# Kernel optimization log

Hardware: AMD Instinct MI355X
Metric: run time of the kernel (lower is better)

Reference implementation:

```python
import jax, jax.numpy as jnp
import numpy as np

B, C, H, W = 8, 192, 120, 120
WSIZES = [4, 8, 12]
BN_EPS = 1e-5


def _conv1x1(t, w, b):
    # t: [b,c,h,w], w: [o,c], b: [o]
    return jnp.einsum('oc,bchw->bohw', w, t) + b[None, :, None, None]


def _bn(t, g, bb, m, v):
    scale = (g * jax.lax.rsqrt(v + BN_EPS))[None, :, None, None]
    return (t - m[None, :, None, None]) * scale + bb[None, :, None, None]


def _partition_qv(t, ws):
    # t: [b, 2c, h, w] -> qx, vx each [b*nh*nw, ws*ws, c]
    b, c2, h, w = t.shape
    c = c2 // 2
    nh, nw = h // ws, w // ws
    t = t.reshape(b, 2, c, nh, ws, nw, ws)
    t = t.transpose(1, 0, 3, 5, 4, 6, 2).reshape(2, b * nh * nw, ws * ws, c)
    return t[0], t[1]


def _merge(t, ws, b, h, w):
    # t: [b*nh*nw, ws*ws, c] -> [b, c, h, w]
    nh, nw = h // ws, w // ws
    c = t.shape[-1]
    t = t.reshape(b, nh, nw, ws, ws, c)
    return t.transpose(0, 5, 1, 3, 2, 4).reshape(b, c, h, w)


def setup_inputs() -> dict:
    key = jax.random.key(0)
    ks = jax.random.split(key, 6)
    d = {}
    d['x'] = jax.random.normal(ks[0], (B, C, H, W), jnp.float32)
    d['y'] = jax.random.normal(ks[1], (B, C, H, W), jnp.float32)
    d['w_in'] = jax.random.normal(ks[2], (2 * C, C), jnp.float32) * 0.05
    d['b_in'] = jax.random.normal(ks[3], (2 * C,), jnp.float32) * 0.01
    d['bn_gamma'] = jnp.ones((2 * C,), jnp.float32)
    d['bn_beta'] = jnp.zeros((2 * C,), jnp.float32)
    d['bn_mean'] = jnp.zeros((2 * C,), jnp.float32)
    d['bn_var'] = jnp.ones((2 * C,), jnp.float32)
    d['w_out'] = jax.random.normal(ks[4], (C, C), jnp.float32) * 0.05
    d['b_out'] = jax.random.normal(ks[5], (C,), jnp.float32) * 0.01
    return d


def reference(x, y, w_in, b_in, bn_gamma, bn_beta, bn_mean, bn_var, w_out, b_out):
    b, c, h, w = x.shape
    xp = _bn(_conv1x1(x, w_in, b_in), bn_gamma, bn_beta, bn_mean, bn_var)
    yp = _bn(_conv1x1(y, w_in, b_in), bn_gamma, bn_beta, bn_mean, bn_var)
    chunk = c * 2 // 3
    y1s, atns = [], []
    for i, ws in enumerate(WSIZES):
        x_ = xp[:, i * chunk:(i + 1) * chunk]
        y_ = yp[:, i * chunk:(i + 1) * chunk]
        s = ws // 2  # shifts > 0 -> shifted windows
        x_ = jnp.roll(x_, (-s, -s), axis=(2, 3))
        y_ = jnp.roll(y_, (-s, -s), axis=(2, 3))
        qx, vx = _partition_qv(x_, ws)
        qy, vy = _partition_qv(y_, ws)
        atn = jax.nn.softmax(jnp.einsum('nqc,nkc->nqk', qx, qy), axis=-1)
        o = jnp.einsum('nqk,nkc->nqc', atn, vx)
        o = _merge(o, ws, b, h, w)
        o = jnp.roll(o, (s, s), axis=(2, 3))
        y1s.append(o)
        atns.append(atn)
    y1 = _conv1x1(jnp.concatenate(y1s, axis=1), w_out, b_out)
    return (y1, atns[0], atns[1], atns[2])
```

## Files before the change

kernel.cpp:

```cpp
#include <hip/hip_runtime.h>

typedef __bf16 bf16x8 __attribute__((ext_vector_type(8)));
typedef float f32x4 __attribute__((ext_vector_type(4)));
typedef float f32x2 __attribute__((ext_vector_type(2)));
typedef unsigned int u32x4 __attribute__((ext_vector_type(4)));
typedef unsigned int u32x2 __attribute__((ext_vector_type(2)));

#define HW 14400
#define CIN 192

__device__ __forceinline__ unsigned short f2bf(float f) {
  unsigned int u = __builtin_bit_cast(unsigned int, f);
  u = (u + 0x7FFFu + ((u >> 16) & 1u)) >> 16;
  return (unsigned short)u;
}
__device__ __forceinline__ float bf2f(unsigned short h) {
  unsigned int u = ((unsigned int)h) << 16;
  return __builtin_bit_cast(float, u);
}

__global__ void prep_kernel(const float* __restrict__ w_in, const float* __restrict__ b_in,
                            const float* __restrict__ g, const float* __restrict__ be,
                            const float* __restrict__ mu, const float* __restrict__ va,
                            const float* __restrict__ w_out,
                            unsigned short* __restrict__ wx, unsigned short* __restrict__ wy,
                            unsigned short* __restrict__ wo,
                            float* __restrict__ bx, float* __restrict__ by) {
  int idx = blockIdx.x * 256 + threadIdx.x;
  if (idx < 384 * 192) {
    int o = idx / 192;
    float s = g[o] * rsqrtf(va[o] + 1e-5f);
    wx[idx] = f2bf(w_in[idx] * s);
  } else if (idx < 384 * 192 + 192 * 192) {
    int j = idx - 384 * 192;
    int jo = j / 192, c = j % 192;
    int o = (jo >> 6) * 128 + (jo & 63);
    float s = g[o] * rsqrtf(va[o] + 1e-5f);
    wy[j] = f2bf(w_in[o * 192 + c] * s);
  } else if (idx < 384 * 192 + 2 * 192 * 192) {
    int j = idx - (384 * 192 + 192 * 192);
    int o = j / 192, cs = j % 192;
    int s = cs & 63;
    int src = (cs & ~63) | ((s & 3) * 16 + (s >> 2));
    wo[j] = f2bf(w_out[o * 192 + src]);
  }
  if (idx < 384) {
    float s = g[idx] * rsqrtf(va[idx] + 1e-5f);
    bx[idx] = (b_in[idx] - mu[idx]) * s + be[idx];
  } else if (idx < 384 + 192) {
    int jo = idx - 384;
    int o = (jo >> 6) * 128 + (jo & 63);
    float s = g[o] * rsqrtf(va[o] + 1e-5f);
    by[jo] = (b_in[o] - mu[o]) * s + be[o];
  }
}

template <int NOUT>
__launch_bounds__(384, 2)
__global__ void conv_in_kernel(const float* __restrict__ X,
                               const unsigned short* __restrict__ Wb,
                               const float* __restrict__ bias,
                               unsigned short* __restrict__ Out) {
  constexpr int M = (NOUT == 384) ? 4 : 2;
  __shared__ unsigned short a_lds[2][64 * 40];
  const int t = threadIdx.x;
  const int wave = t >> 6, lane = t & 63, l15 = lane & 15, l4 = lane >> 4;
  const int wchunk = (NOUT == 384) ? wave : (wave >> 1);
  const int px_base = (NOUT == 384) ? 0 : ((wave & 1) * 32);
  const int wo0 = wchunk * 64;
  const int b = blockIdx.x / 225;
  const int px0 = (blockIdx.x % 225) * 64;
  const float* Xb = X + (size_t)b * CIN * HW + px0;

  f32x4 acc[M][4];
#pragma unroll
  for (int n = 0; n < 4; ++n) {
    float bv = bias[wo0 + n * 16 + l15];
#pragma unroll
    for (int m = 0; m < M; ++m) acc[m][n] = f32x4{bv, bv, bv, bv};
  }

  const int c_off = (t & 7) * 4, px2 = ((t >> 3) & 31) * 2;
  auto stage = [&](int kc, int buf) {
    if (t < 256) {
      const float* src = Xb + (size_t)(kc * 32 + c_off) * HW + px2;
      f32x2 v0 = *reinterpret_cast<const f32x2*>(src);
      f32x2 v1 = *reinterpret_cast<const f32x2*>(src + HW);
      f32x2 v2 = *reinterpret_cast<const f32x2*>(src + 2 * HW);
      f32x2 v3 = *reinterpret_cast<const f32x2*>(src + 3 * HW);
      u32x2 r0 = {(unsigned)f2bf(v0[0]) | ((unsigned)f2bf(v1[0]) << 16),
                  (unsigned)f2bf(v2[0]) | ((unsigned)f2bf(v3[0]) << 16)};
      u32x2 r1 = {(unsigned)f2bf(v0[1]) | ((unsigned)f2bf(v1[1]) << 16),
                  (unsigned)f2bf(v2[1]) | ((unsigned)f2bf(v3[1]) << 16)};
      *reinterpret_cast<u32x2*>(&a_lds[buf][px2 * 40 + c_off]) = r0;
      *reinterpret_cast<u32x2*>(&a_lds[buf][(px2 + 1) * 40 + c_off]) = r1;
    }
  };
  auto loadW = [&](int kc, int n) {
    return *reinterpret_cast<const bf16x8*>(
        Wb + (size_t)(wo0 + n * 16 + l15) * CIN + kc * 32 + l4 * 8);
  };

  stage(0, 0);
  bf16x8 bw[4], bwn[4];
#pragma unroll
  for (int n = 0; n < 4; ++n) bw[n] = loadW(0, n);

  for (int kc = 0; kc < 6; ++kc) {
    __syncthreads();
    if (kc < 5) {
      stage(kc + 1, (kc + 1) & 1);
#pragma unroll
      for (int n = 0; n < 4; ++n) bwn[n] = loadW(kc + 1, n);
    }
    bf16x8 af[M];
#pragma unroll
    for (int m = 0; m < M; ++m)
      af[m] = *reinterpret_cast<const bf16x8*>(
          &a_lds[kc & 1][(px_base + m * 16 + l15) * 40 + l4 * 8]);
#pragma unroll
    for (int n = 0; n < 4; ++n)
#pragma unroll
      for (int m = 0; m < M; ++m)
        acc[m][n] = __builtin_amdgcn_mfma_f32_16x16x32_bf16(af[m], bw[n], acc[m][n], 0, 0, 0);
#pragma unroll
    for (int n = 0; n < 4; ++n) bw[n] = bwn[n];
  }

#pragma unroll
  for (int m = 0; m < M; ++m) {
#pragma unroll
    for (int r = 0; r < 4; ++r) {
      int px = px_base + m * 16 + l4 * 4 + r;
      u32x2 pk = {(unsigned)f2bf(acc[m][0][r]) | ((unsigned)f2bf(acc[m][1][r]) << 16),
                  (unsigned)f2bf(acc[m][2][r]) | ((unsigned)f2bf(acc[m][3][r]) << 16)};
      *reinterpret_cast<u32x2*>(Out + ((size_t)b * HW + px0 + px) * NOUT + wo0 + l15 * 4) = pk;
    }
  }
}

template <int WS, int SI, int NTHR>
__launch_bounds__(NTHR, 2)
__global__ void attn_kernel(const unsigned short* __restrict__ XP,
                            const unsigned short* __restrict__ YQ,
                            unsigned short* __restrict__ Z,
                            float* __restrict__ ATN) {
  constexpr int S = WS / 2, L = WS * WS, NH = 120 / WS, TT = L / 16;
  constexpr int NWAVE = NTHR / 64;
  constexpr int SMAX = (TT + NWAVE - 1) / NWAVE;
  constexpr int KP = ((L + 31) / 32) * 32;
  constexpr int PL = KP + 8;
  constexpr int KSTEPS = KP / 32;
  constexpr int POOLE = (L * 72 > L * PL) ? L * 72 : L * PL;
  __shared__ unsigned short pool[POOLE];
  __shared__ unsigned short vt_lds[64 * PL];
  unsigned short* k_lds = pool;
  unsigned short* p_lds = pool;

  const int t = threadIdx.x;
  const int win = blockIdx.x;
  const int b = win / (NH * NH);
  const int r_ = win % (NH * NH);
  const int ih = r_ / NH, iw = r_ % NH;
  const int wave = t >> 6, lane = t & 63, l15 = lane & 15, l4 = lane >> 4;

  auto pixof = [&](int e) {
    int p = e / WS, qc = e % WS;
    int h = ih * WS + p + S; if (h >= 120) h -= 120;
    int w = iw * WS + qc + S; if (w >= 120) w -= 120;
    return b * HW + h * 120 + w;
  };

  for (int idx = t; idx < L * 8; idx += NTHR) {
    int e = idx >> 3, c8 = (idx & 7) * 8;
    *reinterpret_cast<u32x4*>(&k_lds[e * 72 + c8]) =
        *reinterpret_cast<const u32x4*>(YQ + (size_t)pixof(e) * 192 + SI * 64 + c8);
  }
  for (int idx = t; idx < L * 8; idx += NTHR) {
    int e = idx >> 3, c8 = (idx & 7) * 8;
    u32x4 v = *reinterpret_cast<const u32x4*>(XP + (size_t)pixof(e) * 384 + SI * 128 + 64 + c8);
    const unsigned short* vh = reinterpret_cast<const unsigned short*>(&v);
#pragma unroll
    for (int j = 0; j < 8; ++j) vt_lds[(c8 + j) * PL + e] = vh[j];
  }
  if constexpr (KP > L) {
    for (int idx = t; idx < 64 * (KP - L); idx += NTHR)
      vt_lds[(idx / (KP - L)) * PL + L + (idx % (KP - L))] = 0;
  }

  bf16x8 af[SMAX][2];
#pragma unroll
  for (int si = 0; si < SMAX; ++si) {
    int ti = wave + si * NWAVE;
    if (ti < TT) {
      const unsigned short* qp =
          XP + (size_t)pixof(ti * 16 + l15) * 384 + SI * 128 + l4 * 8;
      af[si][0] = *reinterpret_cast<const bf16x8*>(qp);
      af[si][1] = *reinterpret_cast<const bf16x8*>(qp + 32);
    }
  }
  __syncthreads();

  f32x4 sacc[SMAX][TT];
#pragma unroll
  for (int si = 0; si < SMAX; ++si)
#pragma unroll
    for (int tj = 0; tj < TT; ++tj) sacc[si][tj] = f32x4{0.f, 0.f, 0.f, 0.f};
#pragma unroll
  for (int tj = 0; tj < TT; ++tj) {
    bf16x8 b0 = *reinterpret_cast<const bf16x8*>(&k_lds[(tj * 16 + l15) * 72 + l4 * 8]);
    bf16x8 b1 = *reinterpret_cast<const bf16x8*>(&k_lds[(tj * 16 + l15) * 72 + 32 + l4 * 8]);
#pragma unroll
    for (int si = 0; si < SMAX; ++si) {
      int ti = wave + si * NWAVE;
      if (ti < TT) {
        sacc[si][tj] = __builtin_amdgcn_mfma_f32_16x16x32_bf16(af[si][0], b0, sacc[si][tj], 0, 0, 0);
        sacc[si][tj] = __builtin_amdgcn_mfma_f32_16x16x32_bf16(af[si][1], b1, sacc[si][tj], 0, 0, 0);
      }
    }
  }

  float inv_[SMAX][4];
#pragma unroll
  for (int si = 0; si < SMAX; ++si) {
    int ti = wave + si * NWAVE;
    if (ti < TT) {
#pragma unroll
      for (int r = 0; r < 4; ++r) {
        float m = -1e30f;
#pragma unroll
        for (int tj = 0; tj < TT; ++tj) m = fmaxf(m, sacc[si][tj][r]);
#pragma unroll
        for (int mk = 1; mk < 16; mk <<= 1) m = fmaxf(m, __shfl_xor(m, mk, 64));
        float s = 0.f;
#pragma unroll
        for (int tj = 0; tj < TT; ++tj) {
          float e = __expf(sacc[si][tj][r] - m);
          sacc[si][tj][r] = e;
          s += e;
        }
#pragma unroll
        for (int mk = 1; mk < 16; mk <<= 1) s += __shfl_xor(s, mk, 64);
        inv_[si][r] = 1.f / s;
      }
    }
  }

  __syncthreads();

  if constexpr (KP > L) {
#pragma unroll
    for (int si = 0; si < SMAX; ++si) {
      int ti = wave + si * NWAVE;
      if (ti < TT)
        *reinterpret_cast<unsigned long long*>(
            &p_lds[(ti * 16 + l15) * PL + L + l4 * 4]) = 0ULL;
    }
  }

  float* aout = ATN + (size_t)win * L * L;
#pragma unroll
  for (int si = 0; si < SMAX; ++si) {
    int ti = wave + si * NWAVE;
    if (ti < TT) {
#pragma unroll
      for (int tj = 0; tj < TT; ++tj)
#pragma unroll
        for (int r = 0; r < 4; ++r) {
          float p = sacc[si][tj][r] * inv_[si][r];
          int row = ti * 16 + l4 * 4 + r, col = tj * 16 + l15;
          aout[row * L + col] = p;
          p_lds[row * PL + col] = f2bf(p);
        }
    }
  }
  __syncthreads();

#pragma unroll
  for (int si = 0; si < SMAX; ++si) {
    int ti = wave + si * NWAVE;
    if (ti < TT) {
      bf16x8 ap[KSTEPS];
#pragma unroll
      for (int kk = 0; kk < KSTEPS; ++kk)
        ap[kk] = *reinterpret_cast<const bf16x8*>(&p_lds[(ti * 16 + l15) * PL + kk * 32 + l4 * 8]);
      int opix[4];
#pragma unroll
      for (int r = 0; r < 4; ++r) opix[r] = pixof(ti * 16 + l4 * 4 + r);
#pragma unroll
      for (int cj = 0; cj < 4; ++cj) {
        f32x4 o = {0.f, 0.f, 0.f, 0.f};
#pragma unroll
        for (int kk = 0; kk < KSTEPS; ++kk) {
          bf16x8 bv = *reinterpret_cast<const bf16x8*>(&vt_lds[(cj * 16 + l15) * PL + kk * 32 + l4 * 8]);
          o = __builtin_amdgcn_mfma_f32_16x16x32_bf16(ap[kk], bv, o, 0, 0, 0);
        }
#pragma unroll
        for (int r = 0; r < 4; ++r)
          Z[(size_t)opix[r] * 192 + SI * 64 + cj * 16 + l15] = f2bf(o[r]);
      }
    }
  }
}

__launch_bounds__(256, 2)
__global__ void conv_out_kernel(const unsigned short* __restrict__ Z,
                                const unsigned short* __restrict__ Wo,
                                const float* __restrict__ bout,
                                float* __restrict__ Y1) {
  __shared__ unsigned short z_lds[64 * 40];
  __shared__ unsigned short w_lds[192 * 40];
  __shared__ float ep[4][48 * 68];
  const int t = threadIdx.x, wave = t >> 6, lane = t & 63;
  const int l15 = lane & 15, l4 = lane >> 4;
  const int b = blockIdx.x / 225, px0 = (blockIdx.x % 225) * 64;
  const unsigned short* Zb = Z + ((size_t)b * HW + px0) * 192;
  const int wo0 = wave * 48;
  f32x4 acc[3][4];
#pragma unroll
  for (int m = 0; m < 3; ++m) {
    f32x4 bv;
#pragma unroll
    for (int r = 0; r < 4; ++r) bv[r] = bout[wo0 + m * 16 + l4 * 4 + r];
#pragma unroll
    for (int n = 0; n < 4; ++n) acc[m][n] = bv;
  }
  for (int kc = 0; kc < 6; ++kc) {
    const int c0 = kc * 32;
    {
      int px = t >> 2, c8 = (t & 3) * 8;
      *reinterpret_cast<u32x4*>(&z_lds[px * 40 + c8]) =
          *reinterpret_cast<const u32x4*>(Zb + (size_t)px * 192 + c0 + c8);
    }
#pragma unroll
    for (int p = 0; p < 3; ++p) {
      int o = p * 64 + (t >> 2), c8 = (t & 3) * 8;
      *reinterpret_cast<u32x4*>(&w_lds[o * 40 + c8]) =
          *reinterpret_cast<const u32x4*>(Wo + (size_t)o * 192 + c0 + c8);
    }
    __syncthreads();
    bf16x8 bfr[4];
#pragma unroll
    for (int n = 0; n < 4; ++n)
      bfr[n] = *reinterpret_cast<const bf16x8*>(&z_lds[(n * 16 + l15) * 40 + l4 * 8]);
#pragma unroll
    for (int m = 0; m < 3; ++m) {
      bf16x8 af = *reinterpret_cast<const bf16x8*>(&w_lds[(wo0 + m * 16 + l15) * 40 + l4 * 8]);
#pragma unroll
      for (int n = 0; n < 4; ++n)
        acc[m][n] = __builtin_amdgcn_mfma_f32_16x16x32_bf16(af, bfr[n], acc[m][n], 0, 0, 0);
    }
    __syncthreads();
  }

  float* sl = ep[wave];
#pragma unroll
  for (int m = 0; m < 3; ++m)
#pragma unroll
    for (int n = 0; n < 4; ++n)
#pragma unroll
      for (int r = 0; r < 4; ++r)
        sl[(m * 16 + l4 * 4 + r) * 68 + n * 16 + l15] = acc[m][n][r];

  float* Yb = Y1 + (size_t)b * 192 * HW + px0;
#pragma unroll
  for (int i = 0; i < 3; ++i) {
    int row = i * 16 + (lane >> 2);
    int col0 = (lane & 3) * 16;
#pragma unroll
    for (int q = 0; q < 4; ++q) {
      f32x4 vv = *reinterpret_cast<const f32x4*>(&sl[row * 68 + col0 + q * 4]);
      *reinterpret_cast<f32x4*>(Yb + (size_t)(wo0 + row) * HW + col0 + q * 4) = vv;
    }
  }
}

extern "C" void kernel_launch(void* const* d_in, const int* in_sizes, int n_in,
                              void* d_out, int out_size, void* d_ws, size_t ws_size,
                              hipStream_t stream) {
  const float* x = (const float*)d_in[0];
  const float* y = (const float*)d_in[1];
  const float* w_in = (const float*)d_in[2];
  const float* b_in = (const float*)d_in[3];
  const float* g = (const float*)d_in[4];
  const float* be = (const float*)d_in[5];
  const float* mu = (const float*)d_in[6];
  const float* va = (const float*)d_in[7];
  const float* w_out = (const float*)d_in[8];
  const float* b_out = (const float*)d_in[9];
  char* ws = (char*)d_ws;
  unsigned short* wx = (unsigned short*)(ws + 0);
  unsigned short* wy = (unsigned short*)(ws + 147456);
  unsigned short* wo = (unsigned short*)(ws + 221184);
  float* bx = (float*)(ws + 294912);
  float* by = (float*)(ws + 296448);
  unsigned short* xp = (unsigned short*)(ws + 297216);
  unsigned short* yq = (unsigned short*)(ws + 297216 + (size_t)115200 * 384 * 2);
  unsigned short* z  = (unsigned short*)(ws + 297216 + (size_t)115200 * 384 * 2 +
                                         (size_t)115200 * 192 * 2);
  float* out = (float*)d_out;

  prep_kernel<<<576, 256, 0, stream>>>(w_in, b_in, g, be, mu, va, w_out, wx, wy, wo, bx, by);
  conv_in_kernel<384><<<1800, 384, 0, stream>>>(x, wx, bx, xp);
  conv_in_kernel<192><<<1800, 384, 0, stream>>>(y, wy, by, yq);
  attn_kernel<4, 0, 64><<<7200, 64, 0, stream>>>(xp, yq, z, out + 22118400);
  attn_kernel<8, 1, 256><<<1800, 256, 0, stream>>>(xp, yq, z, out + 23961600);
  attn_kernel<12, 2, 256><<<800, 256, 0, stream>>>(xp, yq, z, out + 31334400);
  conv_out_kernel<<<1800, 256, 0, stream>>>(z, wo, b_out, out);
}
```

Measured before the change: 277.5 us.

## Stage full input tile once in conv_in and drop LDS epilogue in conv_out

conv_in now loads the whole 192-channel by 64-pixel input tile up front with 16-byte vector loads, converts it to bf16 into a single large LDS buffer, and synchronises once. This replaces the per-k-chunk double-buffered staging and its per-iteration barriers. conv_out stops transposing results through an LDS scratch area and writes accumulators directly to global memory in 64-byte row segments. The trade-offs are more LDS and registers per block in conv_in, scalar 2-byte LDS stores that may hit bank conflicts, and less coalesced global stores in conv_out.

```diff
diff --git a/kernel.cpp b/kernel.cpp
--- a/kernel.cpp
+++ b/kernel.cpp
@@ -2,7 +2,6 @@
 
 typedef __bf16 bf16x8 __attribute__((ext_vector_type(8)));
 typedef float f32x4 __attribute__((ext_vector_type(4)));
-typedef float f32x2 __attribute__((ext_vector_type(2)));
 typedef unsigned int u32x4 __attribute__((ext_vector_type(4)));
 typedef unsigned int u32x2 __attribute__((ext_vector_type(2)));
 
@@ -62,7 +61,7 @@
                                const float* __restrict__ bias,
                                unsigned short* __restrict__ Out) {
   constexpr int M = (NOUT == 384) ? 4 : 2;
-  __shared__ unsigned short a_lds[2][64 * 40];
+  __shared__ unsigned short a_lds[64 * 200];
   const int t = threadIdx.x;
   const int wave = t >> 6, lane = t & 63, l15 = lane & 15, l4 = lane >> 4;
   const int wchunk = (NOUT == 384) ? wave : (wave >> 1);
@@ -72,44 +71,44 @@
   const int px0 = (blockIdx.x % 225) * 64;
   const float* Xb = X + (size_t)b * CIN * HW + px0;
 
-  f32x4 acc[M][4];
-#pragma unroll
-  for (int n = 0; n < 4; ++n) {
-    float bv = bias[wo0 + n * 16 + l15];
-#pragma unroll
-    for (int m = 0; m < M; ++m) acc[m][n] = f32x4{bv, bv, bv, bv};
-  }
-
-  const int c_off = (t & 7) * 4, px2 = ((t >> 3) & 31) * 2;
-  auto stage = [&](int kc, int buf) {
-    if (t < 256) {
-      const float* src = Xb + (size_t)(kc * 32 + c_off) * HW + px2;
-      f32x2 v0 = *reinterpret_cast<const f32x2*>(src);
-      f32x2 v1 = *reinterpret_cast<const f32x2*>(src + HW);
-      f32x2 v2 = *reinterpret_cast<const f32x2*>(src + 2 * HW);
-      f32x2 v3 = *reinterpret_cast<const f32x2*>(src + 3 * HW);
-      u32x2 r0 = {(unsigned)f2bf(v0[0]) | ((unsigned)f2bf(v1[0]) << 16),
-                  (unsigned)f2bf(v2[0]) | ((unsigned)f2bf(v3[0]) << 16)};
-      u32x2 r1 = {(unsigned)f2bf(v0[1]) | ((unsigned)f2bf(v1[1]) << 16),
-                  (unsigned)f2bf(v2[1]) | ((unsigned)f2bf(v3[1]) << 16)};
-      *reinterpret_cast<u32x2*>(&a_lds[buf][px2 * 40 + c_off]) = r0;
-      *reinterpret_cast<u32x2*>(&a_lds[buf][(px2 + 1) * 40 + c_off]) = r1;
-    }
-  };
   auto loadW = [&](int kc, int n) {
     return *reinterpret_cast<const bf16x8*>(
         Wb + (size_t)(wo0 + n * 16 + l15) * CIN + kc * 32 + l4 * 8);
   };
 
-  stage(0, 0);
+  f32x4 sv[8];
+#pragma unroll
+  for (int j = 0; j < 8; ++j) {
+    int idx = j * 384 + t;
+    int c = idx >> 4, px4 = (idx & 15) * 4;
+    sv[j] = *reinterpret_cast<const f32x4*>(Xb + (size_t)c * HW + px4);
+  }
   bf16x8 bw[4], bwn[4];
 #pragma unroll
   for (int n = 0; n < 4; ++n) bw[n] = loadW(0, n);
 
+  f32x4 acc[M][4];
+#pragma unroll
+  for (int n = 0; n < 4; ++n) {
+    float bv = bias[wo0 + n * 16 + l15];
+#pragma unroll
+    for (int m = 0; m < M; ++m) acc[m][n] = f32x4{bv, bv, bv, bv};
+  }
+
+#pragma unroll
+  for (int j = 0; j < 8; ++j) {
+    int idx = j * 384 + t;
+    int c = idx >> 4, px4 = (idx & 15) * 4;
+    a_lds[(px4 + 0) * 200 + c] = f2bf(sv[j][0]);
+    a_lds[(px4 + 1) * 200 + c] = f2bf(sv[j][1]);
+    a_lds[(px4 + 2) * 200 + c] = f2bf(sv[j][2]);
+    a_lds[(px4 + 3) * 200 + c] = f2bf(sv[j][3]);
+  }
+  __syncthreads();
+
+#pragma unroll
   for (int kc = 0; kc < 6; ++kc) {
-    __syncthreads();
     if (kc < 5) {
-      stage(kc + 1, (kc + 1) & 1);
 #pragma unroll
       for (int n = 0; n < 4; ++n) bwn[n] = loadW(kc + 1, n);
     }
@@ -117,7 +116,7 @@
 #pragma unroll
     for (int m = 0; m < M; ++m)
       af[m] = *reinterpret_cast<const bf16x8*>(
-          &a_lds[kc & 1][(px_base + m * 16 + l15) * 40 + l4 * 8]);
+          &a_lds[(px_base + m * 16 + l15) * 200 + kc * 32 + l4 * 8]);
 #pragma unroll
     for (int n = 0; n < 4; ++n)
 #pragma unroll
@@ -310,7 +309,6 @@
                                 float* __restrict__ Y1) {
   __shared__ unsigned short z_lds[64 * 40];
   __shared__ unsigned short w_lds[192 * 40];
-  __shared__ float ep[4][48 * 68];
   const int t = threadIdx.x, wave = t >> 6, lane = t & 63;
   const int l15 = lane & 15, l4 = lane >> 4;
   const int b = blockIdx.x / 225, px0 = (blockIdx.x % 225) * 64;
@@ -352,25 +350,15 @@
     }
     __syncthreads();
   }
-
-  float* sl = ep[wave];
-#pragma unroll
-  for (int m = 0; m < 3; ++m)
-#pragma unroll
-    for (int n = 0; n < 4; ++n)
-#pragma unroll
-      for (int r = 0; r < 4; ++r)
-        sl[(m * 16 + l4 * 4 + r) * 68 + n * 16 + l15] = acc[m][n][r];
-
   float* Yb = Y1 + (size_t)b * 192 * HW + px0;
 #pragma unroll
-  for (int i = 0; i < 3; ++i) {
-    int row = i * 16 + (lane >> 2);
-    int col0 = (lane & 3) * 16;
-#pragma unroll
-    for (int q = 0; q < 4; ++q) {
-      f32x4 vv = *reinterpret_cast<const f32x4*>(&sl[row * 68 + col0 + q * 4]);
-      *reinterpret_cast<f32x4*>(Yb + (size_t)(wo0 + row) * HW + col0 + q * 4) = vv;
+  for (int m = 0; m < 3; ++m) {
+#pragma unroll
+    for (int r = 0; r < 4; ++r) {
+      int o = wo0 + m * 16 + l4 * 4 + r;
+      float* dst = Yb + (size_t)o * HW + l15;
+#pragma unroll
+      for (int n = 0; n < 4; ++n) dst[n * 16] = acc[m][n][r];
     }
   }
 }
```

Measured after the change: 253.3 us. 8.7% less time.
